# Optimization experiments

Hardware: AMD Instinct MI355X
Metric: run time of the kernel (lower is better)

## Reference

```python
import jax, jax.numpy as jnp
import numpy as np

D_MODEL = 256
N_HEADS = 8
HEAD_DIM = D_MODEL // N_HEADS  # 32
N_LEVELS = 4
N_POINTS = 4
LEVEL_SHAPES = [(100, 100), (50, 50), (25, 25), (13, 13)]
LEVEL_STARTS = [0] + list(np.cumsum([h * w for h, w in LEVEL_SHAPES]))[:-1]
LEN_IN = int(sum(h * w for h, w in LEVEL_SHAPES))  # 13294
BATCH = 2
LEN_Q = LEN_IN  # encoder self-attention


def _offset_bias():
    # faithful to MSDeformAttn._reset_parameters for sampling_offsets bias
    thetas = np.arange(N_HEADS, dtype=np.float32) * (2.0 * np.pi / N_HEADS)
    grid = np.stack([np.cos(thetas), np.sin(thetas)], -1)
    grid = grid / np.abs(grid).max(-1, keepdims=True)
    grid = np.tile(grid.reshape(N_HEADS, 1, 1, 2), (1, N_LEVELS, N_POINTS, 1))
    for i in range(N_POINTS):
        grid[:, :, i, :] *= i + 1
    return jnp.asarray(grid.reshape(-1), dtype=jnp.float32)


def setup_inputs() -> dict:
    key = jax.random.key(0)
    ks = jax.random.split(key, 10)
    s = 1.0 / np.sqrt(D_MODEL)
    inp = {
        "query": jax.random.normal(ks[0], (BATCH, LEN_Q, D_MODEL), jnp.float32),
        "reference_points": jax.random.uniform(ks[1], (BATCH, LEN_Q, N_LEVELS, 2), jnp.float32),
        "input_flatten": jax.random.normal(ks[2], (BATCH, LEN_IN, D_MODEL), jnp.float32),
        "input_spatial_shapes": jnp.asarray(LEVEL_SHAPES, dtype=jnp.int32),
        "W_value": jax.random.normal(ks[3], (D_MODEL, D_MODEL), jnp.float32) * s,
        "b_value": jnp.zeros((D_MODEL,), jnp.float32),
        "W_off": jax.random.normal(ks[4], (D_MODEL, N_HEADS * N_LEVELS * N_POINTS * 2), jnp.float32) * 0.01,
        "b_off": _offset_bias(),
        "W_attn": jax.random.normal(ks[5], (D_MODEL, N_HEADS * N_LEVELS * N_POINTS), jnp.float32) * 0.01,
        "b_attn": jnp.zeros((N_HEADS * N_LEVELS * N_POINTS,), jnp.float32),
        "W_out": jax.random.normal(ks[6], (D_MODEL, D_MODEL), jnp.float32) * s,
        "b_out": jnp.zeros((D_MODEL,), jnp.float32),
    }
    return inp


def _corner(v_t, ix, iy, h, w):
    # v_t: (n, M, h*w, D); ix/iy: (n, M, LqP) int32. Zero padding outside.
    valid = (ix >= 0) & (ix < w) & (iy >= 0) & (iy < h)
    idx = jnp.clip(iy, 0, h - 1) * w + jnp.clip(ix, 0, w - 1)
    g = jnp.take_along_axis(v_t, idx[..., None], axis=2)  # (n, M, LqP, D)
    return g * valid[..., None].astype(v_t.dtype)


def _ms_deform_attn(query, reference_points, input_flatten,
                    W_value, b_value, W_off, b_off, W_attn, b_attn, W_out, b_out):
    n, lq, _ = query.shape
    value = (input_flatten @ W_value + b_value).reshape(n, LEN_IN, N_HEADS, HEAD_DIM)
    offs = (query @ W_off + b_off).reshape(n, lq, N_HEADS, N_LEVELS, N_POINTS, 2)
    aw = jax.nn.softmax(
        (query @ W_attn + b_attn).reshape(n, lq, N_HEADS, N_LEVELS * N_POINTS), axis=-1
    ).reshape(n, lq, N_HEADS, N_LEVELS, N_POINTS)
    # offset_normalizer = (w, h) per level
    norm = jnp.asarray([[w, h] for h, w in LEVEL_SHAPES], dtype=query.dtype)
    loc = reference_points[:, :, None, :, None, :] + offs / norm[None, None, None, :, None, :]

    acc = jnp.zeros((n, N_HEADS, lq, HEAD_DIM), dtype=value.dtype)
    for l, (h, w) in enumerate(LEVEL_SHAPES):
        s0 = LEVEL_STARTS[l]
        v_t = jnp.transpose(value[:, s0:s0 + h * w], (0, 2, 1, 3))  # (n, M, hw, D)
        ll = loc[:, :, :, l]  # (n, lq, M, P, 2) in [0,1]
        # grid_sample bilinear, align_corners=False: pixel = coord*size - 0.5
        x = ll[..., 0] * w - 0.5
        y = ll[..., 1] * h - 0.5
        x0 = jnp.floor(x); y0 = jnp.floor(y)
        tx = x - x0; ty = y - y0
        ix0 = x0.astype(jnp.int32); iy0 = y0.astype(jnp.int32)
        flat = lambda a: jnp.transpose(a, (0, 2, 1, 3)).reshape(n, N_HEADS, lq * N_POINTS)
        ix0f, iy0f = flat(ix0), flat(iy0)
        txf = flat(tx)[..., None]; tyf = flat(ty)[..., None]
        g00 = _corner(v_t, ix0f, iy0f, h, w)
        g01 = _corner(v_t, ix0f + 1, iy0f, h, w)
        g10 = _corner(v_t, ix0f, iy0f + 1, h, w)
        g11 = _corner(v_t, ix0f + 1, iy0f + 1, h, w)
        samp = (g00 * (1 - txf) * (1 - tyf) + g01 * txf * (1 - tyf)
                + g10 * (1 - txf) * tyf + g11 * txf * tyf)
        samp = samp.reshape(n, N_HEADS, lq, N_POINTS, HEAD_DIM)
        wl = jnp.transpose(aw[:, :, :, l], (0, 2, 1, 3))[..., None]  # (n, M, lq, P, 1)
        acc = acc + (samp * wl).sum(axis=3)

    out = jnp.transpose(acc, (0, 2, 1, 3)).reshape(n, lq, D_MODEL)
    return out @ W_out + b_out


def reference(query, reference_points, input_flatten, input_spatial_shapes,
              W_value, b_value, W_off, b_off, W_attn, b_attn, W_out, b_out):
    # input_spatial_shapes carried for signature fidelity; level geometry is static.
    return _ms_deform_attn(query, reference_points, input_flatten,
                           W_value, b_value, W_off, b_off, W_attn, b_attn, W_out, b_out)
```

## Files before the change

### kernel.cpp

```cpp
#include <hip/hip_runtime.h>

#define NH 8
#define HD 32
#define NL 4
#define NP 4
#define DM 256
#define LEN_IN_C 13294
#define LQ_C 13294
#define B_C 2
#define M_TOTAL (B_C * LQ_C)
#define MT_TILES 1662
#define RT32_TILES 831
#define GQ 32
#define QBLKS 831

typedef __attribute__((ext_vector_type(8))) short short8;
typedef __attribute__((ext_vector_type(4))) float floatx4;

__device__ __forceinline__ unsigned short f2bf(float x) {
    union { float f; unsigned int u; } a; a.f = x;
    unsigned int r = (a.u + 0x7FFFu + ((a.u >> 16) & 1u)) >> 16;
    return (unsigned short)r;
}
__device__ __forceinline__ unsigned short f2h(float x) {
    unsigned int r;
    asm("v_cvt_f16_f32 %0, %1" : "=v"(r) : "v"(x));
    return (unsigned short)r;
}
__device__ __forceinline__ unsigned int cvtpk_bf16(float lo, float hi) {
    unsigned int r;
    asm("v_cvt_pk_bf16_f32 %0, %1, %2" : "=v"(r) : "v"(lo), "v"(hi));
    return r;
}

#define FMAMIX_LO(acc, v, w) \
    asm("v_fma_mix_f32 %0, %1, %2, %0 op_sel_hi:[1,0,0]" : "+v"(acc) : "v"(v), "v"(w))
#define FMAMIX_HI(acc, v, w) \
    asm("v_fma_mix_f32 %0, %1, %2, %0 op_sel:[1,0,0] op_sel_hi:[1,0,0]" : "+v"(acc) : "v"(v), "v"(w))

__device__ __forceinline__ void conv_b_body(const float* __restrict__ W,
                                            unsigned short* __restrict__ Bsw,
                                            int Nsrc, int NTsrc, int NTtotal, int ntOff,
                                            int vblk) {
    const int u = vblk * 256 + threadIdx.x;
    const int lane = u & 63;
    const int unit = u >> 6;
    const int ntl = unit % NTsrc;
    const int kc = unit / NTsrc;
    const int n = ntl * 16 + (lane & 15);
    const int k0 = kc * 32 + (lane >> 4) * 8;
    short8 v;
#pragma unroll
    for (int j = 0; j < 8; ++j)
        v[j] = (short)f2bf(W[(size_t)(k0 + j) * Nsrc + n]);
    ((short8*)Bsw)[(size_t)(kc * NTtotal + ntOff + ntl) * 64 + lane] = v;
}

__global__ __launch_bounds__(256) void conv_weights_kernel(const float* __restrict__ Wv,
                                                           const float* __restrict__ Woff,
                                                           const float* __restrict__ Wattn,
                                                           const float* __restrict__ Wout,
                                                           const float* __restrict__ boff,
                                                           const float* __restrict__ battn,
                                                           unsigned short* __restrict__ BswV,
                                                           unsigned short* __restrict__ BswOA,
                                                           unsigned short* __restrict__ BswO,
                                                           float* __restrict__ fbias,
                                                           unsigned short* __restrict__ value,
                                                           unsigned short* __restrict__ AccSw) {
    const int blk = blockIdx.x;
    if (blk < 32)        conv_b_body(Wv,    BswV,  256, 16, 16, 0,  blk);
    else if (blk < 64)   conv_b_body(Woff,  BswOA, 256, 16, 24, 0,  blk - 32);
    else if (blk < 80)   conv_b_body(Wattn, BswOA, 128,  8, 24, 16, blk - 64);
    else if (blk < 112)  conv_b_body(Wout,  BswO,  256, 16, 16, 0,  blk - 80);
    else if (blk < 114) {
        const int t = (blk - 112) * 256 + threadIdx.x;
        if (t < 384) fbias[t] = (t < 256) ? boff[t] : battn[t - 256];
        else if (t < 416) {
            const int j = t - 384;
            value[-32 + j] = 0;
            value[(size_t)M_TOTAL * 256 + j] = 0;
        }
    } else {
        const int idx = threadIdx.x;
        if (idx < 128) {
            const int kc = idx >> 4;
            const int sub = idx & 15;
            const int lane = (12 + (sub & 3)) + 16 * (sub >> 2);
            const size_t unit = (size_t)(1661 * 8 + kc) * 64 + lane;
            short8 z = (short8){0, 0, 0, 0, 0, 0, 0, 0};
            ((short8*)AccSw)[unit] = z;
        }
    }
}

template <int NT, int OUTMODE, int RT>
__device__ __forceinline__ void gemm_lds_full(unsigned short* __restrict__ sA,
                                              const float* __restrict__ A,
                                              const unsigned short* __restrict__ Bsw,
                                              const float* __restrict__ bias,
                                              void* __restrict__ Cout, int M, int rtb) {
    constexpr int NTW = NT / 4;
    constexpr int ROWS = RT * 16;
    const int tid = threadIdx.x;
    const int lane = tid & 63;
    const int wave = tid >> 6;
    const int trow = rtb * ROWS;

#pragma unroll
    for (int i = 0; i < RT * 4; ++i) {
        const int li = i * 1024 + tid * 4;
        const int lrow = li >> 8;
        const int lcol = li & 255;
        const int srow = min(trow + lrow, M - 1);
        const float4 f = *(const float4*)(A + (size_t)srow * 256 + lcol);
        uint2 pk;
        pk.x = cvtpk_bf16(f.x, f.y);
        pk.y = cvtpk_bf16(f.z, f.w);
        const int lb = (li * 2) ^ ((lrow & 7) << 4);
        *(uint2*)((char*)sA + lb) = pk;
    }
    __syncthreads();

    const int m = lane & 15;
    const int q = lane >> 4;
    const short8* Bu = (const short8*)Bsw;

    floatx4 acc[RT][NTW];
#pragma unroll
    for (int r = 0; r < RT; ++r)
#pragma unroll
        for (int t = 0; t < NTW; ++t) acc[r][t] = (floatx4){0.f, 0.f, 0.f, 0.f};

    const int swz = (m & 7) << 4;
#pragma unroll 2
    for (int kc = 0; kc < 8; ++kc) {
        short8 a[RT];
#pragma unroll
        for (int r = 0; r < RT; ++r) {
            const int fb = ((m + r * 16) * 512 + kc * 64 + q * 16) ^ swz;
            a[r] = *(const short8*)((const char*)sA + fb);
        }
#pragma unroll
        for (int t = 0; t < NTW; ++t) {
            const short8 b = Bu[(size_t)(kc * NT + wave * NTW + t) * 64 + lane];
#pragma unroll
            for (int r = 0; r < RT; ++r)
                acc[r][t] = __builtin_amdgcn_mfma_f32_16x16x32_bf16(a[r], b, acc[r][t], 0, 0, 0);
        }
    }

    const int N = NT * 16;
    const int colq = lane & 15;
    const int rowq = (lane >> 4) * 4;
#pragma unroll
    for (int t = 0; t < NTW; ++t) {
        const int col = (wave * NTW + t) * 16 + colq;
        const float bc = bias[col];
#pragma unroll
        for (int r = 0; r < RT; ++r) {
#pragma unroll
            for (int reg = 0; reg < 4; ++reg) {
                const int row = trow + r * 16 + rowq + reg;
                if (row < M) {
                    const float v = acc[r][t][reg] + bc;
                    if (OUTMODE == 1) {
                        const int bb = row >= LEN_IN_C;
                        const int pos = row - (bb ? LEN_IN_C : 0);
                        const int hh = col >> 5;
                        const int dd = col & 31;
                        ((unsigned short*)Cout)[((size_t)((bb << 3) + hh) * LEN_IN_C + pos) * 32 + dd] = f2h(v);
                    } else {
                        ((float*)Cout)[(size_t)row * N + col] = v;
                    }
                }
            }
        }
    }
}

__global__ __launch_bounds__(256) void front_gemm_kernel(const float* __restrict__ inflat,
                                                         const float* __restrict__ query,
                                                         const unsigned short* __restrict__ BswV,
                                                         const unsigned short* __restrict__ BswOA,
                                                         const float* __restrict__ bv,
                                                         const float* __restrict__ fbias,
                                                         unsigned short* __restrict__ value,
                                                         float* __restrict__ fused, int M) {
    __shared__ unsigned short sA[32 * 256];
    const int x = blockIdx.x;
    const int rt32 = x >> 1;
    if ((x & 1) == 0)
        gemm_lds_full<16, 1, 2>(sA, inflat, BswV, bv, (void*)value, M, rt32);
    else
        gemm_lds_full<24, 0, 2>(sA, query, BswOA, fbias, (void*)fused, M, rt32);
}

__global__ __launch_bounds__(256) void back_gemm_kernel(const unsigned short* __restrict__ Asw,
                                                        const unsigned short* __restrict__ Bsw,
                                                        const float* __restrict__ bias,
                                                        float* __restrict__ Cout, int M) {
    constexpr int NT = 16;
    constexpr int NTW = 4;
    const int tid = threadIdx.x;
    const int lane = tid & 63;
    const int wave = tid >> 6;
    const int rt = blockIdx.x;

    const short8* Au = (const short8*)Asw;
    const short8* Bu = (const short8*)Bsw;

    floatx4 acc[NTW];
#pragma unroll
    for (int t = 0; t < NTW; ++t) acc[t] = (floatx4){0.f, 0.f, 0.f, 0.f};

#pragma unroll 2
    for (int kc = 0; kc < 8; ++kc) {
        const short8 a = Au[(size_t)(rt * 8 + kc) * 64 + lane];
#pragma unroll
        for (int t = 0; t < NTW; ++t) {
            const short8 b = Bu[(size_t)(kc * NT + wave * NTW + t) * 64 + lane];
            acc[t] = __builtin_amdgcn_mfma_f32_16x16x32_bf16(a, b, acc[t], 0, 0, 0);
        }
    }

    const int colq = lane & 15;
    const int rowq = (lane >> 4) * 4;
#pragma unroll
    for (int t = 0; t < NTW; ++t) {
        const int col = (wave * NTW + t) * 16 + colq;
        const float bc = bias[col];
#pragma unroll
        for (int reg = 0; reg < 4; ++reg) {
            const int row = rt * 16 + rowq + reg;
            if (row < M)
                Cout[(size_t)row * 256 + col] = acc[t][reg] + bc;
        }
    }
}

__global__ __launch_bounds__(256, 8) void msda_sample_kernel(const float* __restrict__ refp,
                                                             const unsigned short* __restrict__ value,
                                                             const float* __restrict__ fused,
                                                             unsigned short* __restrict__ AccSw) {
    constexpr int lvl_hw[4] = {100, 50, 25, 13};
    constexpr int lvl_s[4] = {0, 10000, 12500, 13125};

    const int wg = blockIdx.x;
    const int h = wg & 7;
    const int q0 = (wg >> 3) * GQ;
    const int tid = threadIdx.x;

    __shared__ float s_ref[GQ * 8];
    __shared__ uint4 s_pd[2][GQ * 17];

    s_ref[tid] = refp[min(q0 * 8 + tid, M_TOTAL * 8 - 1)];
    __syncthreads();

#pragma unroll
    for (int jj = 0; jj < 2; ++jj) {
        const int job = jj * 256 + tid;
        const int qq = job >> 4;
        const int t16 = job & 15;
        const int l = t16 >> 2;
        const int bq = min(q0 + qq, M_TOTAL - 1);
        const int b = (bq >= LQ_C) ? 1 : 0;

        const float logit = fused[(size_t)bq * 384 + 256 + h * 16 + t16];
        float m = logit;
#pragma unroll
        for (int mask = 1; mask < 16; mask <<= 1) m = fmaxf(m, __shfl_xor(m, mask));
        const float e = expf(logit - m);
        float s = e;
#pragma unroll
        for (int mask = 1; mask < 16; mask <<= 1) s += __shfl_xor(s, mask);
        const float aw = e / s;

        const int whl = lvl_hw[l];
        const float fwh = (float)whl;
        const float2 oxy = *(const float2*)(fused + (size_t)bq * 384 + (h * 16 + t16) * 2);
        const float x = s_ref[qq * 8 + l * 2] * fwh + oxy.x - 0.5f;
        const float y = s_ref[qq * 8 + l * 2 + 1] * fwh + oxy.y - 0.5f;
        const float x0f = floorf(x), y0f = floorf(y);
        const float tx = x - x0f, ty = y - y0f;
        const int ix0 = (int)x0f, iy0 = (int)y0f;

        const bool xv0 = (unsigned)ix0 < (unsigned)whl;
        const bool xv1 = (unsigned)(ix0 + 1) < (unsigned)whl;
        const bool yv0 = (unsigned)iy0 < (unsigned)whl;
        const bool yv1 = (unsigned)(iy0 + 1) < (unsigned)whl;

        const int cxp = min(max(ix0, -1), whl - 1);
        const int cy0 = min(max(iy0, 0), whl - 1);
        const int cy1 = min(max(iy0 + 1, 0), whl - 1);

        const int posb = (b * 8 + h) * LEN_IN_C + lvl_s[l];
        const int offT = (posb + cy0 * whl + cxp) * 64;
        const int offB = (posb + cy1 * whl + cxp) * 64;
        const float w00 = (xv0 && yv0) ? aw * (1.f - tx) * (1.f - ty) : 0.f;
        const float w01 = (xv1 && yv0) ? aw * tx * (1.f - ty) : 0.f;
        const float w10 = (xv0 && yv1) ? aw * (1.f - tx) * ty : 0.f;
        const float w11 = (xv1 && yv1) ? aw * tx * ty : 0.f;
        const int slot = qq * 17 + t16;
        uint4 d0, d1;
        d0.x = (unsigned)offT; d0.y = (unsigned)offB;
        d0.z = __float_as_uint(w00); d0.w = __float_as_uint(w10);
        d1.x = (unsigned)offT; d1.y = (unsigned)offB;
        d1.z = __float_as_uint(w01); d1.w = __float_as_uint(w11);
        s_pd[0][slot] = d0;
        s_pd[1][slot] = d1;
    }
    __syncthreads();

    const int qq = tid >> 3;
    const int l8 = tid & 7;
    const char* vbp = (const char*)value + l8 * 16;
    const int pbase = qq * 17;
    const int side = (l8 >> 2) & 1;

    float a0 = 0.f, a1 = 0.f, a2 = 0.f, a3 = 0.f;
    float a4 = 0.f, a5 = 0.f, a6 = 0.f, a7 = 0.f;
#pragma unroll 2
    for (int pt = 0; pt < 16; ++pt) {
        const uint4 d = s_pd[side][pbase + pt];
        const float wt = __uint_as_float(d.z);
        const float wb = __uint_as_float(d.w);
        const uint4 vt = *(const uint4*)(vbp + (int)d.x);
        const uint4 vb = *(const uint4*)(vbp + (int)d.y);
        FMAMIX_LO(a0, vt.x, wt); FMAMIX_HI(a1, vt.x, wt);
        FMAMIX_LO(a2, vt.y, wt); FMAMIX_HI(a3, vt.y, wt);
        FMAMIX_LO(a4, vt.z, wt); FMAMIX_HI(a5, vt.z, wt);
        FMAMIX_LO(a6, vt.w, wt); FMAMIX_HI(a7, vt.w, wt);
        FMAMIX_LO(a0, vb.x, wb); FMAMIX_HI(a1, vb.x, wb);
        FMAMIX_LO(a2, vb.y, wb); FMAMIX_HI(a3, vb.y, wb);
        FMAMIX_LO(a4, vb.z, wb); FMAMIX_HI(a5, vb.z, wb);
        FMAMIX_LO(a6, vb.w, wb); FMAMIX_HI(a7, vb.w, wb);
    }

    a0 += __shfl_xor(a0, 4); a1 += __shfl_xor(a1, 4);
    a2 += __shfl_xor(a2, 4); a3 += __shfl_xor(a3, 4);
    a4 += __shfl_xor(a4, 4); a5 += __shfl_xor(a5, 4);
    a6 += __shfl_xor(a6, 4); a7 += __shfl_xor(a7, 4);

    const int bq = q0 + qq;
    if (side == 0 && bq < M_TOTAL) {
        const int rt = bq >> 4, mm = bq & 15;
        const int unit = (rt * 8 + h) * 64 + ((l8 & 3) * 16 + mm);
        uint4 o;
        o.x = cvtpk_bf16(a0, a1);
        o.y = cvtpk_bf16(a2, a3);
        o.z = cvtpk_bf16(a4, a5);
        o.w = cvtpk_bf16(a6, a7);
        *(uint4*)(AccSw + (size_t)unit * 8) = o;
    }
}

extern "C" void kernel_launch(void* const* d_in, const int* in_sizes, int n_in,
                              void* d_out, int out_size, void* d_ws, size_t ws_size,
                              hipStream_t stream) {
    const float* query  = (const float*)d_in[0];
    const float* refp   = (const float*)d_in[1];
    const float* inflat = (const float*)d_in[2];
    const float* Wv    = (const float*)d_in[4];
    const float* bv    = (const float*)d_in[5];
    const float* Woff  = (const float*)d_in[6];
    const float* boff  = (const float*)d_in[7];
    const float* Wattn = (const float*)d_in[8];
    const float* battn = (const float*)d_in[9];
    const float* Wout  = (const float*)d_in[10];
    const float* bout  = (const float*)d_in[11];
    float* out = (float*)d_out;

    char* p = (char*)d_ws;
    unsigned short* AccSw = (unsigned short*)p;
    p += (size_t)MT_TILES * 8 * 64 * 8 * sizeof(unsigned short);
    unsigned short* BswV = (unsigned short*)p;   p += (size_t)8 * 16 * 64 * 8 * 2;
    unsigned short* BswOA = (unsigned short*)p;  p += (size_t)8 * 24 * 64 * 8 * 2;
    unsigned short* BswO = (unsigned short*)p;   p += (size_t)8 * 16 * 64 * 8 * 2;
    float* fbias = (float*)p;                    p += 384 * sizeof(float);
    unsigned short* value = (unsigned short*)p + 32;
    p += ((size_t)M_TOTAL * 256 + 64) * sizeof(unsigned short);
    float* fused = (float*)p;                    p += (size_t)M_TOTAL * 384 * 4;

    const int M = M_TOTAL;

    conv_weights_kernel<<<115, 256, 0, stream>>>(Wv, Woff, Wattn, Wout, boff, battn,
                                                 BswV, BswOA, BswO, fbias, value, AccSw);
    front_gemm_kernel<<<RT32_TILES * 2, 256, 0, stream>>>(inflat, query, BswV, BswOA,
                                                          bv, fbias, value, fused, M);
    msda_sample_kernel<<<QBLKS * 8, 256, 0, stream>>>(refp, value, fused, AccSw);
    back_gemm_kernel<<<MT_TILES, 256, 0, stream>>>(AccSw, BswO, bout, out, M);
}
```

Measured before the change: 201.1 us.

## Software-pipeline GEMM operand loads and batch gathers in sampling kernel

The front GEMM now double-buffers B fragments from global memory and A fragments from LDS, so loads for the next K chunk are issued before the current MFMAs run. The back GEMM gives each block two 16-row tiles, halving the grid and reusing each B fragment across both tiles, with the same double buffering. The sampling kernel gathers four points' value vectors at a time into double-buffered registers to keep more loads in flight, and its launch bound drops from 8 to 4 blocks per CU to leave room for the extra registers. The cost is more register pressure and possibly lower occupancy. Note that MT_TILES is 1662, so the back-GEMM grid of 831 blocks covers every tile.

```diff
diff --git a/kernel.cpp b/kernel.cpp
--- a/kernel.cpp
+++ b/kernel.cpp
@@ -94,21 +94,20 @@
     }
 }
 
-template <int NT, int OUTMODE, int RT>
-__device__ __forceinline__ void gemm_lds_full(unsigned short* __restrict__ sA,
+template <int NT, int OUTMODE>
+__device__ __forceinline__ void gemm_lds_pipe(unsigned short* __restrict__ sA,
                                               const float* __restrict__ A,
                                               const unsigned short* __restrict__ Bsw,
                                               const float* __restrict__ bias,
-                                              void* __restrict__ Cout, int M, int rtb) {
+                                              void* __restrict__ Cout, int M, int rt32) {
     constexpr int NTW = NT / 4;
-    constexpr int ROWS = RT * 16;
     const int tid = threadIdx.x;
     const int lane = tid & 63;
     const int wave = tid >> 6;
-    const int trow = rtb * ROWS;
-
-#pragma unroll
-    for (int i = 0; i < RT * 4; ++i) {
+    const int trow = rt32 * 32;
+
+#pragma unroll
+    for (int i = 0; i < 8; ++i) {
         const int li = i * 1024 + tid * 4;
         const int lrow = li >> 8;
         const int lcol = li & 255;
@@ -125,28 +124,37 @@
     const int m = lane & 15;
     const int q = lane >> 4;
     const short8* Bu = (const short8*)Bsw;
-
-    floatx4 acc[RT][NTW];
-#pragma unroll
-    for (int r = 0; r < RT; ++r)
+    const int swz = (m & 7) << 4;
+
+    floatx4 acc[2][NTW];
+#pragma unroll
+    for (int r = 0; r < 2; ++r)
 #pragma unroll
         for (int t = 0; t < NTW; ++t) acc[r][t] = (floatx4){0.f, 0.f, 0.f, 0.f};
 
-    const int swz = (m & 7) << 4;
-#pragma unroll 2
+    short8 br[2][NTW];
+    short8 ar[2][2];
+#pragma unroll
+    for (int t = 0; t < NTW; ++t)
+        br[0][t] = Bu[(size_t)(0 * NT + wave * NTW + t) * 64 + lane];
+    ar[0][0] = *(const short8*)((const char*)sA + ((m * 512 + 0 * 64 + q * 16) ^ swz));
+    ar[0][1] = *(const short8*)((const char*)sA + (((m + 16) * 512 + 0 * 64 + q * 16) ^ swz));
+
+#pragma unroll
     for (int kc = 0; kc < 8; ++kc) {
-        short8 a[RT];
-#pragma unroll
-        for (int r = 0; r < RT; ++r) {
-            const int fb = ((m + r * 16) * 512 + kc * 64 + q * 16) ^ swz;
-            a[r] = *(const short8*)((const char*)sA + fb);
+        const int cur = kc & 1;
+        const int nxt = cur ^ 1;
+        if (kc < 7) {
+#pragma unroll
+            for (int t = 0; t < NTW; ++t)
+                br[nxt][t] = Bu[(size_t)((kc + 1) * NT + wave * NTW + t) * 64 + lane];
+            ar[nxt][0] = *(const short8*)((const char*)sA + ((m * 512 + (kc + 1) * 64 + q * 16) ^ swz));
+            ar[nxt][1] = *(const short8*)((const char*)sA + (((m + 16) * 512 + (kc + 1) * 64 + q * 16) ^ swz));
         }
 #pragma unroll
         for (int t = 0; t < NTW; ++t) {
-            const short8 b = Bu[(size_t)(kc * NT + wave * NTW + t) * 64 + lane];
-#pragma unroll
-            for (int r = 0; r < RT; ++r)
-                acc[r][t] = __builtin_amdgcn_mfma_f32_16x16x32_bf16(a[r], b, acc[r][t], 0, 0, 0);
+            acc[0][t] = __builtin_amdgcn_mfma_f32_16x16x32_bf16(ar[cur][0], br[cur][t], acc[0][t], 0, 0, 0);
+            acc[1][t] = __builtin_amdgcn_mfma_f32_16x16x32_bf16(ar[cur][1], br[cur][t], acc[1][t], 0, 0, 0);
         }
     }
 
@@ -158,7 +166,7 @@
         const int col = (wave * NTW + t) * 16 + colq;
         const float bc = bias[col];
 #pragma unroll
-        for (int r = 0; r < RT; ++r) {
+        for (int r = 0; r < 2; ++r) {
 #pragma unroll
             for (int reg = 0; reg < 4; ++reg) {
                 const int row = trow + r * 16 + rowq + reg;
@@ -191,9 +199,9 @@
     const int x = blockIdx.x;
     const int rt32 = x >> 1;
     if ((x & 1) == 0)
-        gemm_lds_full<16, 1, 2>(sA, inflat, BswV, bv, (void*)value, M, rt32);
+        gemm_lds_pipe<16, 1>(sA, inflat, BswV, bv, (void*)value, M, rt32);
     else
-        gemm_lds_full<24, 0, 2>(sA, query, BswOA, fbias, (void*)fused, M, rt32);
+        gemm_lds_pipe<24, 0>(sA, query, BswOA, fbias, (void*)fused, M, rt32);
 }
 
 __global__ __launch_bounds__(256) void back_gemm_kernel(const unsigned short* __restrict__ Asw,
@@ -205,22 +213,40 @@
     const int tid = threadIdx.x;
     const int lane = tid & 63;
     const int wave = tid >> 6;
-    const int rt = blockIdx.x;
+    const int rt0 = blockIdx.x * 2;
 
     const short8* Au = (const short8*)Asw;
     const short8* Bu = (const short8*)Bsw;
 
-    floatx4 acc[NTW];
-#pragma unroll
-    for (int t = 0; t < NTW; ++t) acc[t] = (floatx4){0.f, 0.f, 0.f, 0.f};
-
-#pragma unroll 2
+    floatx4 acc[2][NTW];
+#pragma unroll
+    for (int r = 0; r < 2; ++r)
+#pragma unroll
+        for (int t = 0; t < NTW; ++t) acc[r][t] = (floatx4){0.f, 0.f, 0.f, 0.f};
+
+    short8 br[2][NTW];
+    short8 ar[2][2];
+#pragma unroll
+    for (int t = 0; t < NTW; ++t)
+        br[0][t] = Bu[(size_t)(0 * NT + wave * NTW + t) * 64 + lane];
+    ar[0][0] = Au[(size_t)(rt0 * 8 + 0) * 64 + lane];
+    ar[0][1] = Au[(size_t)((rt0 + 1) * 8 + 0) * 64 + lane];
+
+#pragma unroll
     for (int kc = 0; kc < 8; ++kc) {
-        const short8 a = Au[(size_t)(rt * 8 + kc) * 64 + lane];
+        const int cur = kc & 1;
+        const int nxt = cur ^ 1;
+        if (kc < 7) {
+#pragma unroll
+            for (int t = 0; t < NTW; ++t)
+                br[nxt][t] = Bu[(size_t)((kc + 1) * NT + wave * NTW + t) * 64 + lane];
+            ar[nxt][0] = Au[(size_t)(rt0 * 8 + kc + 1) * 64 + lane];
+            ar[nxt][1] = Au[(size_t)((rt0 + 1) * 8 + kc + 1) * 64 + lane];
+        }
 #pragma unroll
         for (int t = 0; t < NTW; ++t) {
-            const short8 b = Bu[(size_t)(kc * NT + wave * NTW + t) * 64 + lane];
-            acc[t] = __builtin_amdgcn_mfma_f32_16x16x32_bf16(a, b, acc[t], 0, 0, 0);
+            acc[0][t] = __builtin_amdgcn_mfma_f32_16x16x32_bf16(ar[cur][0], br[cur][t], acc[0][t], 0, 0, 0);
+            acc[1][t] = __builtin_amdgcn_mfma_f32_16x16x32_bf16(ar[cur][1], br[cur][t], acc[1][t], 0, 0, 0);
         }
     }
 
@@ -231,15 +257,18 @@
         const int col = (wave * NTW + t) * 16 + colq;
         const float bc = bias[col];
 #pragma unroll
-        for (int reg = 0; reg < 4; ++reg) {
-            const int row = rt * 16 + rowq + reg;
-            if (row < M)
-                Cout[(size_t)row * 256 + col] = acc[t][reg] + bc;
-        }
-    }
-}
-
-__global__ __launch_bounds__(256, 8) void msda_sample_kernel(const float* __restrict__ refp,
+        for (int r = 0; r < 2; ++r) {
+#pragma unroll
+            for (int reg = 0; reg < 4; ++reg) {
+                const int row = (rt0 + r) * 16 + rowq + reg;
+                if (row < M)
+                    Cout[(size_t)row * 256 + col] = acc[r][t][reg] + bc;
+            }
+        }
+    }
+}
+
+__global__ __launch_bounds__(256, 4) void msda_sample_kernel(const float* __restrict__ refp,
                                                              const unsigned short* __restrict__ value,
                                                              const float* __restrict__ fused,
                                                              unsigned short* __restrict__ AccSw) {
@@ -315,26 +344,49 @@
     const int qq = tid >> 3;
     const int l8 = tid & 7;
     const char* vbp = (const char*)value + l8 * 16;
-    const int pbase = qq * 17;
     const int side = (l8 >> 2) & 1;
+    const uint4* pd = &s_pd[side][qq * 17];
+
+    uint4 dsc[2][4];
+    uint4 vt[2][4], vb[2][4];
+#pragma unroll
+    for (int j = 0; j < 4; ++j) dsc[0][j] = pd[j];
+#pragma unroll
+    for (int j = 0; j < 4; ++j) {
+        vt[0][j] = *(const uint4*)(vbp + (int)dsc[0][j].x);
+        vb[0][j] = *(const uint4*)(vbp + (int)dsc[0][j].y);
+    }
 
     float a0 = 0.f, a1 = 0.f, a2 = 0.f, a3 = 0.f;
     float a4 = 0.f, a5 = 0.f, a6 = 0.f, a7 = 0.f;
-#pragma unroll 2
-    for (int pt = 0; pt < 16; ++pt) {
-        const uint4 d = s_pd[side][pbase + pt];
-        const float wt = __uint_as_float(d.z);
-        const float wb = __uint_as_float(d.w);
-        const uint4 vt = *(const uint4*)(vbp + (int)d.x);
-        const uint4 vb = *(const uint4*)(vbp + (int)d.y);
-        FMAMIX_LO(a0, vt.x, wt); FMAMIX_HI(a1, vt.x, wt);
-        FMAMIX_LO(a2, vt.y, wt); FMAMIX_HI(a3, vt.y, wt);
-        FMAMIX_LO(a4, vt.z, wt); FMAMIX_HI(a5, vt.z, wt);
-        FMAMIX_LO(a6, vt.w, wt); FMAMIX_HI(a7, vt.w, wt);
-        FMAMIX_LO(a0, vb.x, wb); FMAMIX_HI(a1, vb.x, wb);
-        FMAMIX_LO(a2, vb.y, wb); FMAMIX_HI(a3, vb.y, wb);
-        FMAMIX_LO(a4, vb.z, wb); FMAMIX_HI(a5, vb.z, wb);
-        FMAMIX_LO(a6, vb.w, wb); FMAMIX_HI(a7, vb.w, wb);
+#pragma unroll
+    for (int c = 0; c < 4; ++c) {
+        const int cur = c & 1;
+        const int nxt = cur ^ 1;
+        if (c < 3) {
+#pragma unroll
+            for (int j = 0; j < 4; ++j) dsc[nxt][j] = pd[(c + 1) * 4 + j];
+#pragma unroll
+            for (int j = 0; j < 4; ++j) {
+                vt[nxt][j] = *(const uint4*)(vbp + (int)dsc[nxt][j].x);
+                vb[nxt][j] = *(const uint4*)(vbp + (int)dsc[nxt][j].y);
+            }
+        }
+#pragma unroll
+        for (int j = 0; j < 4; ++j) {
+            const float wt = __uint_as_float(dsc[cur][j].z);
+            const float wb = __uint_as_float(dsc[cur][j].w);
+            const uint4 t4 = vt[cur][j];
+            const uint4 b4 = vb[cur][j];
+            FMAMIX_LO(a0, t4.x, wt); FMAMIX_HI(a1, t4.x, wt);
+            FMAMIX_LO(a2, t4.y, wt); FMAMIX_HI(a3, t4.y, wt);
+            FMAMIX_LO(a4, t4.z, wt); FMAMIX_HI(a5, t4.z, wt);
+            FMAMIX_LO(a6, t4.w, wt); FMAMIX_HI(a7, t4.w, wt);
+            FMAMIX_LO(a0, b4.x, wb); FMAMIX_HI(a1, b4.x, wb);
+            FMAMIX_LO(a2, b4.y, wb); FMAMIX_HI(a3, b4.y, wb);
+            FMAMIX_LO(a4, b4.z, wb); FMAMIX_HI(a5, b4.z, wb);
+            FMAMIX_LO(a6, b4.w, wb); FMAMIX_HI(a7, b4.w, wb);
+        }
     }
 
     a0 += __shfl_xor(a0, 4); a1 += __shfl_xor(a1, 4);
@@ -389,5 +441,5 @@
     front_gemm_kernel<<<RT32_TILES * 2, 256, 0, stream>>>(inflat, query, BswV, BswOA,
                                                           bv, fbias, value, fused, M);
     msda_sample_kernel<<<QBLKS * 8, 256, 0, stream>>>(refp, value, fused, AccSw);
-    back_gemm_kernel<<<MT_TILES, 256, 0, stream>>>(AccSw, BswO, bout, out, M);
-}
+    back_gemm_kernel<<<RT32_TILES, 256, 0, stream>>>(AccSw, BswO, bout, out, M);
+}
```

After: 198.3 us. Within noise of the previous version (-1.4%).

## Use direct global-to-LDS loads of fp32 rows and split GEMM tiles finer

Applied to the files above, without the earlier changes.

The front GEMM now stages fp32 activation rows straight into padded LDS with global_load_lds instead of converting to bf16 in registers first. Tiles shrink from 32 to 16 rows, so the grid doubles and the bf16 conversion moves into the MFMA inner loop. The back GEMM splits each 16-row tile's N dimension across two blocks for more parallelism, and the softmax uses the fast __expf. The trade-off is reloading B fragments per smaller tile, extra conversion work per k-step, and the slightly less accurate exponential.

```diff
diff --git a/kernel.cpp b/kernel.cpp
--- a/kernel.cpp
+++ b/kernel.cpp
@@ -10,9 +10,9 @@
 #define B_C 2
 #define M_TOTAL (B_C * LQ_C)
 #define MT_TILES 1662
-#define RT32_TILES 831
 #define GQ 32
 #define QBLKS 831
+#define LROWB 1040
 
 typedef __attribute__((ext_vector_type(8))) short short8;
 typedef __attribute__((ext_vector_type(4))) float floatx4;
@@ -37,6 +37,12 @@
     asm("v_fma_mix_f32 %0, %1, %2, %0 op_sel_hi:[1,0,0]" : "+v"(acc) : "v"(v), "v"(w))
 #define FMAMIX_HI(acc, v, w) \
     asm("v_fma_mix_f32 %0, %1, %2, %0 op_sel:[1,0,0] op_sel_hi:[1,0,0]" : "+v"(acc) : "v"(v), "v"(w))
+
+__device__ __forceinline__ void dma16(const float* g, float* l) {
+    __builtin_amdgcn_global_load_lds(
+        (const __attribute__((address_space(1))) unsigned int*)(g),
+        (__attribute__((address_space(3))) unsigned int*)(l), 16, 0, 0);
+}
 
 __device__ __forceinline__ void conv_b_body(const float* __restrict__ W,
                                             unsigned short* __restrict__ Bsw,
@@ -94,59 +100,34 @@
     }
 }
 
-template <int NT, int OUTMODE, int RT>
-__device__ __forceinline__ void gemm_lds_full(unsigned short* __restrict__ sA,
-                                              const float* __restrict__ A,
-                                              const unsigned short* __restrict__ Bsw,
-                                              const float* __restrict__ bias,
-                                              void* __restrict__ Cout, int M, int rtb) {
+template <int NT, int OUTMODE>
+__device__ __forceinline__ void tile_compute_f32lds(const float* __restrict__ sA,
+                                                    const unsigned short* __restrict__ Bsw,
+                                                    const float* __restrict__ bias,
+                                                    void* __restrict__ Cout, int M, int trow,
+                                                    int lane, int wave) {
     constexpr int NTW = NT / 4;
-    constexpr int ROWS = RT * 16;
-    const int tid = threadIdx.x;
-    const int lane = tid & 63;
-    const int wave = tid >> 6;
-    const int trow = rtb * ROWS;
-
-#pragma unroll
-    for (int i = 0; i < RT * 4; ++i) {
-        const int li = i * 1024 + tid * 4;
-        const int lrow = li >> 8;
-        const int lcol = li & 255;
-        const int srow = min(trow + lrow, M - 1);
-        const float4 f = *(const float4*)(A + (size_t)srow * 256 + lcol);
-        uint2 pk;
-        pk.x = cvtpk_bf16(f.x, f.y);
-        pk.y = cvtpk_bf16(f.z, f.w);
-        const int lb = (li * 2) ^ ((lrow & 7) << 4);
-        *(uint2*)((char*)sA + lb) = pk;
-    }
-    __syncthreads();
-
     const int m = lane & 15;
     const int q = lane >> 4;
     const short8* Bu = (const short8*)Bsw;
 
-    floatx4 acc[RT][NTW];
-#pragma unroll
-    for (int r = 0; r < RT; ++r)
-#pragma unroll
-        for (int t = 0; t < NTW; ++t) acc[r][t] = (floatx4){0.f, 0.f, 0.f, 0.f};
-
-    const int swz = (m & 7) << 4;
+    floatx4 acc[NTW];
+#pragma unroll
+    for (int t = 0; t < NTW; ++t) acc[t] = (floatx4){0.f, 0.f, 0.f, 0.f};
+
 #pragma unroll 2
     for (int kc = 0; kc < 8; ++kc) {
-        short8 a[RT];
-#pragma unroll
-        for (int r = 0; r < RT; ++r) {
-            const int fb = ((m + r * 16) * 512 + kc * 64 + q * 16) ^ swz;
-            a[r] = *(const short8*)((const char*)sA + fb);
-        }
+        const char* fb = (const char*)sA + m * LROWB + kc * 128 + q * 32;
+        const float4 f0 = *(const float4*)fb;
+        const float4 f1 = *(const float4*)(fb + 16);
+        union { uint4 u; short8 s; } c;
+        c.u.x = cvtpk_bf16(f0.x, f0.y); c.u.y = cvtpk_bf16(f0.z, f0.w);
+        c.u.z = cvtpk_bf16(f1.x, f1.y); c.u.w = cvtpk_bf16(f1.z, f1.w);
+        const short8 a = c.s;
 #pragma unroll
         for (int t = 0; t < NTW; ++t) {
             const short8 b = Bu[(size_t)(kc * NT + wave * NTW + t) * 64 + lane];
-#pragma unroll
-            for (int r = 0; r < RT; ++r)
-                acc[r][t] = __builtin_amdgcn_mfma_f32_16x16x32_bf16(a[r], b, acc[r][t], 0, 0, 0);
+            acc[t] = __builtin_amdgcn_mfma_f32_16x16x32_bf16(a, b, acc[t], 0, 0, 0);
         }
     }
 
@@ -158,21 +139,18 @@
         const int col = (wave * NTW + t) * 16 + colq;
         const float bc = bias[col];
 #pragma unroll
-        for (int r = 0; r < RT; ++r) {
-#pragma unroll
-            for (int reg = 0; reg < 4; ++reg) {
-                const int row = trow + r * 16 + rowq + reg;
-                if (row < M) {
-                    const float v = acc[r][t][reg] + bc;
-                    if (OUTMODE == 1) {
-                        const int bb = row >= LEN_IN_C;
-                        const int pos = row - (bb ? LEN_IN_C : 0);
-                        const int hh = col >> 5;
-                        const int dd = col & 31;
-                        ((unsigned short*)Cout)[((size_t)((bb << 3) + hh) * LEN_IN_C + pos) * 32 + dd] = f2h(v);
-                    } else {
-                        ((float*)Cout)[(size_t)row * N + col] = v;
-                    }
+        for (int reg = 0; reg < 4; ++reg) {
+            const int row = trow + rowq + reg;
+            if (row < M) {
+                const float v = acc[t][reg] + bc;
+                if (OUTMODE == 1) {
+                    const int bb = row >= LEN_IN_C;
+                    const int pos = row - (bb ? LEN_IN_C : 0);
+                    const int hh = col >> 5;
+                    const int dd = col & 31;
+                    ((unsigned short*)Cout)[((size_t)((bb << 3) + hh) * LEN_IN_C + pos) * 32 + dd] = f2h(v);
+                } else {
+                    ((float*)Cout)[(size_t)row * N + col] = v;
                 }
             }
         }
@@ -187,39 +165,55 @@
                                                          const float* __restrict__ fbias,
                                                          unsigned short* __restrict__ value,
                                                          float* __restrict__ fused, int M) {
-    __shared__ unsigned short sA[32 * 256];
+    __shared__ float sA[16 * LROWB / 4];
+    const int tid = threadIdx.x;
+    const int lane = tid & 63;
+    const int wave = tid >> 6;
     const int x = blockIdx.x;
-    const int rt32 = x >> 1;
-    if ((x & 1) == 0)
-        gemm_lds_full<16, 1, 2>(sA, inflat, BswV, bv, (void*)value, M, rt32);
+    const int flavor = x & 1;
+    const int trow = (x >> 1) * 16;
+    const float* A = flavor ? query : inflat;
+
+#pragma unroll
+    for (int i = 0; i < 4; ++i) {
+        const int lrow = i * 4 + wave;
+        const int srow = min(trow + lrow, M - 1);
+        dma16(A + (size_t)srow * 256 + lane * 4,
+              (float*)((char*)sA + lrow * LROWB));
+    }
+    __syncthreads();
+
+    if (flavor == 0)
+        tile_compute_f32lds<16, 1>(sA, BswV, bv, (void*)value, M, trow, lane, wave);
     else
-        gemm_lds_full<24, 0, 2>(sA, query, BswOA, fbias, (void*)fused, M, rt32);
+        tile_compute_f32lds<24, 0>(sA, BswOA, fbias, (void*)fused, M, trow, lane, wave);
 }
 
 __global__ __launch_bounds__(256) void back_gemm_kernel(const unsigned short* __restrict__ Asw,
                                                         const unsigned short* __restrict__ Bsw,
                                                         const float* __restrict__ bias,
                                                         float* __restrict__ Cout, int M) {
-    constexpr int NT = 16;
-    constexpr int NTW = 4;
     const int tid = threadIdx.x;
     const int lane = tid & 63;
     const int wave = tid >> 6;
-    const int rt = blockIdx.x;
+    const int x = blockIdx.x;
+    const int rt = x >> 1;
+    const int half = x & 1;
+    const int nt0 = half * 8 + wave * 2;
 
     const short8* Au = (const short8*)Asw;
     const short8* Bu = (const short8*)Bsw;
 
-    floatx4 acc[NTW];
-#pragma unroll
-    for (int t = 0; t < NTW; ++t) acc[t] = (floatx4){0.f, 0.f, 0.f, 0.f};
+    floatx4 acc[2];
+    acc[0] = (floatx4){0.f, 0.f, 0.f, 0.f};
+    acc[1] = acc[0];
 
 #pragma unroll 2
     for (int kc = 0; kc < 8; ++kc) {
         const short8 a = Au[(size_t)(rt * 8 + kc) * 64 + lane];
 #pragma unroll
-        for (int t = 0; t < NTW; ++t) {
-            const short8 b = Bu[(size_t)(kc * NT + wave * NTW + t) * 64 + lane];
+        for (int t = 0; t < 2; ++t) {
+            const short8 b = Bu[(size_t)(kc * 16 + nt0 + t) * 64 + lane];
             acc[t] = __builtin_amdgcn_mfma_f32_16x16x32_bf16(a, b, acc[t], 0, 0, 0);
         }
     }
@@ -227,8 +221,8 @@
     const int colq = lane & 15;
     const int rowq = (lane >> 4) * 4;
 #pragma unroll
-    for (int t = 0; t < NTW; ++t) {
-        const int col = (wave * NTW + t) * 16 + colq;
+    for (int t = 0; t < 2; ++t) {
+        const int col = (nt0 + t) * 16 + colq;
         const float bc = bias[col];
 #pragma unroll
         for (int reg = 0; reg < 4; ++reg) {
@@ -270,7 +264,7 @@
         float m = logit;
 #pragma unroll
         for (int mask = 1; mask < 16; mask <<= 1) m = fmaxf(m, __shfl_xor(m, mask));
-        const float e = expf(logit - m);
+        const float e = __expf(logit - m);
         float s = e;
 #pragma unroll
         for (int mask = 1; mask < 16; mask <<= 1) s += __shfl_xor(s, mask);
@@ -386,8 +380,8 @@
 
     conv_weights_kernel<<<115, 256, 0, stream>>>(Wv, Woff, Wattn, Wout, boff, battn,
                                                  BswV, BswOA, BswO, fbias, value, AccSw);
-    front_gemm_kernel<<<RT32_TILES * 2, 256, 0, stream>>>(inflat, query, BswV, BswOA,
-                                                          bv, fbias, value, fused, M);
+    front_gemm_kernel<<<MT_TILES * 2, 256, 0, stream>>>(inflat, query, BswV, BswOA,
+                                                        bv, fbias, value, fused, M);
     msda_sample_kernel<<<QBLKS * 8, 256, 0, stream>>>(refp, value, fused, AccSw);
-    back_gemm_kernel<<<MT_TILES, 256, 0, stream>>>(AccSw, BswO, bout, out, M);
-}
+    back_gemm_kernel<<<MT_TILES * 2, 256, 0, stream>>>(AccSw, BswO, bout, out, M);
+}
```

Result: faster. 196.1 us (-2.5%).
